# Kernel optimization log

Hardware: AMD Instinct MI355X
Metric: run time of the kernel (lower is better)

The kernel has to match this reference:

```python
import jax, jax.numpy as jnp
import numpy as np

B, C, D = 32, 24, 12          # batch, feature channels, spatial grid
Q_DIM = 11                    # hardcoded question dim in original (k*2+11)
K = C + 2                     # channels after coordinate concat
G_IN = 2 * K + Q_DIM          # 63
G_HID = 256
F_OUT = 10


def setup_inputs() -> dict:
    key = jax.random.key(0)
    ks = jax.random.split(key, 7)
    s = lambda fan_in: 1.0 / np.sqrt(fan_in)
    return {
        "image": jax.random.normal(ks[0], (B, C, D, D), jnp.float32),
        "question": jax.random.normal(ks[1], (B, Q_DIM), jnp.float32),
        "Wg1": jax.random.normal(ks[2], (G_IN, G_HID), jnp.float32) * s(G_IN),
        "bg1": jnp.zeros((G_HID,), jnp.float32),
        "Wg2": jax.random.normal(ks[3], (G_HID, G_HID), jnp.float32) * s(G_HID),
        "bg2": jnp.zeros((G_HID,), jnp.float32),
        "Wf1": jax.random.normal(ks[4], (G_HID, G_HID), jnp.float32) * s(G_HID),
        "bf1": jnp.zeros((G_HID,), jnp.float32),
        "Wf2": jax.random.normal(ks[5], (G_HID, F_OUT), jnp.float32) * s(G_HID),
        "bf2": jnp.zeros((F_OUT,), jnp.float32),
    }


def reference(image, question, Wg1, bg1, Wg2, bg2, Wf1, bf1, Wf2, bf2):
    b, c, d, _ = image.shape
    # coordinate channels: torch.arange(0, 1+1e-5, 1/(d-1)) == linspace(0,1,d)
    coord = jnp.linspace(0.0, 1.0, d, dtype=image.dtype)
    cx = jnp.broadcast_to(coord[None, None, None, :], (b, 1, d, d))
    cy = jnp.broadcast_to(coord[None, None, :, None], (b, 1, d, d))
    x = jnp.concatenate([image, cx, cy], axis=1)            # [b, k, d, d]
    k = c + 2
    n = d * d
    x = x.reshape(b, k, n).transpose(0, 2, 1)                # [b, n, k] objects
    # all-pairs construction: left repeats objects along axis 1, right along axis 2
    x_left = jnp.broadcast_to(x[:, None, :, :], (b, n, n, k)).reshape(b, n * n, k)
    x_right = jnp.broadcast_to(x[:, :, None, :], (b, n, n, k)).reshape(b, n * n, k)
    q = jnp.broadcast_to(question[:, None, :], (b, n * n, question.shape[1]))
    pairs = jnp.concatenate([x_left, x_right, q], axis=2)    # [b, n^2, 2k+11]
    # shared MLP g per pair
    h = jax.nn.relu(jnp.einsum('bpi,ih->bph', pairs, Wg1) + bg1)
    h = jax.nn.relu(jnp.einsum('bph,ho->bpo', h, Wg2) + bg2)
    s = h.sum(axis=1)                                        # [b, 256] sum over pairs
    # MLP f
    o = jax.nn.relu(s @ Wf1 + bf1)
    return o @ Wf2 + bf2                                     # [b, 10]
```

## Files before the change

kernel.cpp:

```cpp
#include <hip/hip_runtime.h>
#include <hip/hip_bf16.h>

#define NB   32
#define NC   24
#define ND   12
#define NN   144
#define QD   11
#define GH   256
#define FOUT 10

typedef unsigned short u16;
typedef __attribute__((ext_vector_type(8))) short bf16x8;
typedef __attribute__((ext_vector_type(4))) float f32x4;

#define LQ_U16  0
#define R_U16   1179648
#define BS_U16  2359296
#define S_BYTE  4849664

__device__ inline float b2f(u16 v) {
  union { unsigned u; float f; } c; c.u = ((unsigned)v) << 16; return c.f;
}
__device__ inline u16 f2b(float f) {
  __hip_bfloat16 h = __float2bfloat16(f);
  return *reinterpret_cast<u16*>(&h);
}

__global__ __launch_bounds__(256) void prep(const float* __restrict__ image,
                                            const float* __restrict__ question,
                                            const float* __restrict__ Wg1,
                                            const float* __restrict__ bg1,
                                            const float* __restrict__ Wg2,
                                            u16* __restrict__ Lq,
                                            u16* __restrict__ R,
                                            float* __restrict__ S,
                                            u16* __restrict__ Bswz) {
  int blk = blockIdx.x;
  int h   = threadIdx.x;
  if (blk < 2 * NB * NN) {
    int p     = blk % NN;
    int rest2 = blk / NN;
    int b     = rest2 & (NB - 1);
    int which = rest2 >> 5;
    const float* Wrow = Wg1 + which * (NC + 2) * GH;
    const float* img  = image + b * (NC * NN) + p;
    float acc = 0.f;
#pragma unroll
    for (int c = 0; c < NC; ++c) acc += img[c * NN] * Wrow[c * GH + h];
    int i = p / ND, j = p - i * ND;
    const float inv = 1.0f / (ND - 1);
    acc += (j * inv) * Wrow[24 * GH + h];
    acc += (i * inv) * Wrow[25 * GH + h];
    if (which == 0) {
      acc += bg1[h];
#pragma unroll
      for (int tq = 0; tq < QD; ++tq)
        acc += question[b * QD + tq] * Wg1[(2 * (NC + 2) + tq) * GH + h];
      Lq[(b * NN + p) * GH + h] = f2b(acc);
    } else {
      R[(b * NN + p) * GH + h] = f2b(acc);
    }
  } else {
    int tid = (blk - 2 * NB * NN) * 256 + h;
    int e   = tid & 7;
    int l   = (tid >> 3) & 63;
    int fid = tid >> 9;
    int kt  = fid >> 4, nt = fid & 15;
    int k = kt * 32 + ((l >> 4) << 3) + e;
    int n = (nt << 4) + (l & 15);
    Bswz[tid] = f2b(Wg2[k * GH + n]);
    if (tid < NB * GH) S[tid] = 0.f;
  }
}

__global__ __launch_bounds__(512, 2) void pair_gemm(const u16* __restrict__ Lq,
                                                    const u16* __restrict__ R,
                                                    const u16* __restrict__ Bswz,
                                                    const float* __restrict__ bg2,
                                                    float* __restrict__ S) {
  const int bid = blockIdx.x;
  const int xcd = bid & 7;
  const int idx = bid >> 3;
  const int b   = xcd * 4 + (idx >> 4);
  const int bi  = idx & 15;
  const int t0  = bi * 10 + (bi < 2 ? bi : 2);
  const int cnt = 10 + (bi < 2 ? 1 : 0);

  __shared__ __align__(16) u16 As[8 * 8 * 64 * 8];

  const int t = threadIdx.x;
  const int w = t >> 6, l = t & 63;
  const int wn = w & 3, wm = w >> 2;
  const int brow = t >> 2;
  const int oc   = t & 3;
  const int mf_w   = brow >> 4;
  const int lane_w = ((brow & 15) | (oc << 4)) ^ (oc << 1);
  const int lane_r = l ^ (((l >> 4) & 3) << 1);

  const u16* Lbase = Lq + b * NN * GH;
  const u16* Rbase = R + b * NN * GH;
  const u16* Bl    = Bswz + l * 8;

  float bgv[4];
#pragma unroll
  for (int nt = 0; nt < 4; ++nt)
    bgv[nt] = bg2[(wn << 6) + (nt << 4) + (l & 15)];
  float ssum[4] = {0.f, 0.f, 0.f, 0.f};

  for (int tt = 0; tt < cnt; ++tt) {
    {
      int p = (t0 + tt) * 128 + brow;
      int i = p / NN, j = p - i * NN;
      const u16* Lr = Lbase + i * GH + oc * 8;
      const u16* Rr = Rbase + j * GH + oc * 8;
#pragma unroll
      for (int half = 0; half < 2; ++half) {
        bf16x8 lv[4], rv[4];
#pragma unroll
        for (int q = 0; q < 4; ++q) {
          lv[q] = *(const bf16x8*)(Lr + ((half << 2) | q) * 32);
          rv[q] = *(const bf16x8*)(Rr + ((half << 2) | q) * 32);
        }
#pragma unroll
        for (int q = 0; q < 4; ++q) {
          const int kt = (half << 2) | q;
          u16 o[8];
#pragma unroll
          for (int e = 0; e < 8; ++e) {
            float v = b2f((u16)lv[q][e]) + b2f((u16)rv[q][e]);
            o[e] = f2b(v > 0.f ? v : 0.f);
          }
          *(bf16x8*)&As[((((kt << 3) | mf_w) << 6) | lane_w) << 3] =
              *(bf16x8*)o;
        }
      }
    }
    __syncthreads();

    f32x4 acc[4][4] = {};
#pragma unroll
    for (int kt = 0; kt < 8; ++kt) {
      bf16x8 af[4];
#pragma unroll
      for (int mf = 0; mf < 4; ++mf)
        af[mf] = *(const bf16x8*)
            &As[((((kt << 3) | (wm << 2) | mf) << 6) | lane_r) << 3];
      bf16x8 bfr[4];
#pragma unroll
      for (int nt = 0; nt < 4; ++nt) {
        int fid = (kt << 4) | (wn << 2) | nt;
        bfr[nt] = *(const bf16x8*)(Bl + ((size_t)fid << 9));
      }
      __builtin_amdgcn_s_setprio(1);
#pragma unroll
      for (int mf = 0; mf < 4; ++mf)
#pragma unroll
        for (int nt = 0; nt < 4; ++nt)
          acc[mf][nt] = __builtin_amdgcn_mfma_f32_16x16x32_bf16(
              af[mf], bfr[nt], acc[mf][nt], 0, 0, 0);
      __builtin_amdgcn_s_setprio(0);
    }
#pragma unroll
    for (int nt = 0; nt < 4; ++nt) {
      float s = 0.f;
#pragma unroll
      for (int mf = 0; mf < 4; ++mf)
#pragma unroll
        for (int r = 0; r < 4; ++r) {
          float v = acc[mf][nt][r] + bgv[nt];
          s += v > 0.f ? v : 0.f;
        }
      ssum[nt] += s;
    }
    __syncthreads();
  }

  float* Sb = S + b * GH;
#pragma unroll
  for (int nt = 0; nt < 4; ++nt) {
    float s = ssum[nt];
    s += __shfl_xor(s, 16, 64);
    s += __shfl_xor(s, 32, 64);
    if (l < 16) atomicAdd(&Sb[(wn << 6) + (nt << 4) + l], s);
  }
}

__global__ __launch_bounds__(256) void final_mlp(const float* __restrict__ S,
                                                 const float* __restrict__ Wf1,
                                                 const float* __restrict__ bf1,
                                                 const float* __restrict__ Wf2,
                                                 const float* __restrict__ bf2,
                                                 float* __restrict__ out) {
  __shared__ float sS[GH];
  __shared__ float oS[GH];
  int b = blockIdx.x, h = threadIdx.x;
  sS[h] = S[b * GH + h];
  __syncthreads();
  float acc = bf1[h];
#pragma unroll 8
  for (int k = 0; k < GH; ++k) acc += sS[k] * Wf1[k * GH + h];
  oS[h] = acc > 0.f ? acc : 0.f;
  __syncthreads();
  if (h < FOUT) {
    float o = bf2[h];
#pragma unroll 8
    for (int k = 0; k < GH; ++k) o += oS[k] * Wf2[k * FOUT + h];
    out[b * FOUT + h] = o;
  }
}

extern "C" void kernel_launch(void* const* d_in, const int* in_sizes, int n_in,
                              void* d_out, int out_size, void* d_ws, size_t ws_size,
                              hipStream_t stream) {
  const float* image    = (const float*)d_in[0];
  const float* question = (const float*)d_in[1];
  const float* Wg1      = (const float*)d_in[2];
  const float* bg1      = (const float*)d_in[3];
  const float* Wg2      = (const float*)d_in[4];
  const float* bg2      = (const float*)d_in[5];
  const float* Wf1      = (const float*)d_in[6];
  const float* bf1      = (const float*)d_in[7];
  const float* Wf2      = (const float*)d_in[8];
  const float* bf2      = (const float*)d_in[9];
  float* out = (float*)d_out;

  u16*   wsb  = (u16*)d_ws;
  u16*   Lqp  = wsb + LQ_U16;
  u16*   Rp   = wsb + R_U16;
  u16*   Bswz = wsb + BS_U16;
  float* Sp   = (float*)((char*)d_ws + S_BYTE);

  prep<<<2 * NB * NN + 256, 256, 0, stream>>>(image, question, Wg1, bg1, Wg2,
                                              Lqp, Rp, Sp, Bswz);
  pair_gemm<<<512, 512, 0, stream>>>(Lqp, Rp, Bswz, bg2, Sp);
  final_mlp<<<NB, 256, 0, stream>>>(Sp, Wf1, bf1, Wf2, bf2, out);
}
```

Before: 112.4 us.

## Switch pair GEMM to 32x32x16 MFMA with register-resident Wg2 fragments

Replaces the 16x16x32 MFMA tiling with 32x32x16 bf16 MFMA, so each wave keeps a 2x2 grid of 32x32 accumulators. Each wave's slice of the swizzled Wg2 is loaded once into registers instead of being re-read from global every tile. To match, the Wg2 swizzle layout and the LDS A-tile layout change, and the grid halves to 256 blocks that each process twice as many tiles. The aim is fewer B loads and higher MFMA efficiency, at the cost of much higher register pressure (occupancy 1 block per CU) and fewer blocks than CUs.

```diff
diff --git a/kernel.cpp b/kernel.cpp
--- a/kernel.cpp
+++ b/kernel.cpp
@@ -12,6 +12,7 @@
 typedef unsigned short u16;
 typedef __attribute__((ext_vector_type(8))) short bf16x8;
 typedef __attribute__((ext_vector_type(4))) float f32x4;
+typedef __attribute__((ext_vector_type(16))) float f32x16;
 
 #define LQ_U16  0
 #define R_U16   1179648
@@ -64,16 +65,16 @@
     int tid = (blk - 2 * NB * NN) * 256 + h;
     int e   = tid & 7;
     int l   = (tid >> 3) & 63;
-    int fid = tid >> 9;
-    int kt  = fid >> 4, nt = fid & 15;
-    int k = kt * 32 + ((l >> 4) << 3) + e;
-    int n = (nt << 4) + (l & 15);
+    int f   = tid >> 9;
+    int ks  = f >> 3, nf = f & 7;
+    int k = ks * 16 + ((l >> 5) << 3) + e;
+    int n = (nf << 5) + (l & 31);
     Bswz[tid] = f2b(Wg2[k * GH + n]);
     if (tid < NB * GH) S[tid] = 0.f;
   }
 }
 
-__global__ __launch_bounds__(512, 2) void pair_gemm(const u16* __restrict__ Lq,
+__global__ __launch_bounds__(512, 1) void pair_gemm(const u16* __restrict__ Lq,
                                                     const u16* __restrict__ R,
                                                     const u16* __restrict__ Bswz,
                                                     const float* __restrict__ bg2,
@@ -81,107 +82,104 @@
   const int bid = blockIdx.x;
   const int xcd = bid & 7;
   const int idx = bid >> 3;
-  const int b   = xcd * 4 + (idx >> 4);
-  const int bi  = idx & 15;
-  const int t0  = bi * 10 + (bi < 2 ? bi : 2);
-  const int cnt = 10 + (bi < 2 ? 1 : 0);
-
-  __shared__ __align__(16) u16 As[8 * 8 * 64 * 8];
+  const int b   = xcd * 4 + (idx >> 3);
+  const int bi  = idx & 7;
+  const int t0  = bi * 20 + (bi < 2 ? bi : 2);
+  const int cnt = 20 + (bi < 2 ? 1 : 0);
+
+  __shared__ __align__(16) u16 As[16 * 4 * 64 * 8];
 
   const int t = threadIdx.x;
   const int w = t >> 6, l = t & 63;
   const int wn = w & 3, wm = w >> 2;
   const int brow = t >> 2;
   const int oc   = t & 3;
-  const int mf_w   = brow >> 4;
-  const int lane_w = ((brow & 15) | (oc << 4)) ^ (oc << 1);
-  const int lane_r = l ^ (((l >> 4) & 3) << 1);
 
   const u16* Lbase = Lq + b * NN * GH;
   const u16* Rbase = R + b * NN * GH;
   const u16* Bl    = Bswz + l * 8;
 
-  float bgv[4];
-#pragma unroll
-  for (int nt = 0; nt < 4; ++nt)
-    bgv[nt] = bg2[(wn << 6) + (nt << 4) + (l & 15)];
-  float ssum[4] = {0.f, 0.f, 0.f, 0.f};
+  bf16x8 bq[2][16];
+#pragma unroll
+  for (int j = 0; j < 2; ++j)
+#pragma unroll
+    for (int ks = 0; ks < 16; ++ks)
+      bq[j][ks] = *(const bf16x8*)
+          (Bl + ((size_t)((ks << 3) | (wn << 1) | j) << 9));
+
+  float bgv[2];
+#pragma unroll
+  for (int j = 0; j < 2; ++j)
+    bgv[j] = bg2[(wn << 6) + (j << 5) + (l & 31)];
+  float ssum[2] = {0.f, 0.f};
 
   for (int tt = 0; tt < cnt; ++tt) {
     {
       int p = (t0 + tt) * 128 + brow;
       int i = p / NN, j = p - i * NN;
-      const u16* Lr = Lbase + i * GH + oc * 8;
-      const u16* Rr = Rbase + j * GH + oc * 8;
-#pragma unroll
-      for (int half = 0; half < 2; ++half) {
-        bf16x8 lv[4], rv[4];
-#pragma unroll
-        for (int q = 0; q < 4; ++q) {
-          lv[q] = *(const bf16x8*)(Lr + ((half << 2) | q) * 32);
-          rv[q] = *(const bf16x8*)(Rr + ((half << 2) | q) * 32);
+      const u16* Lr = Lbase + i * GH;
+      const u16* Rr = Rbase + j * GH;
+#pragma unroll
+      for (int u = 0; u < 8; ++u) {
+        const int ko = oc + (u << 2);
+        bf16x8 lv = *(const bf16x8*)(Lr + ko * 8);
+        bf16x8 rv = *(const bf16x8*)(Rr + ko * 8);
+        u16 o[8];
+#pragma unroll
+        for (int e = 0; e < 8; ++e) {
+          float v = b2f((u16)lv[e]) + b2f((u16)rv[e]);
+          o[e] = f2b(v > 0.f ? v : 0.f);
         }
-#pragma unroll
-        for (int q = 0; q < 4; ++q) {
-          const int kt = (half << 2) | q;
-          u16 o[8];
-#pragma unroll
-          for (int e = 0; e < 8; ++e) {
-            float v = b2f((u16)lv[q][e]) + b2f((u16)rv[q][e]);
-            o[e] = f2b(v > 0.f ? v : 0.f);
-          }
-          *(bf16x8*)&As[((((kt << 3) | mf_w) << 6) | lane_w) << 3] =
-              *(bf16x8*)o;
-        }
+        const int ks = ko >> 1;
+        const int kb = ko & 1;
+        const int mf = brow >> 5;
+        const int pl = ((kb << 5) | (brow & 31)) ^ (oc << 1);
+        *(bf16x8*)&As[((((ks << 2) | mf) << 6) | pl) << 3] = *(bf16x8*)o;
       }
     }
     __syncthreads();
 
-    f32x4 acc[4][4] = {};
-#pragma unroll
-    for (int kt = 0; kt < 8; ++kt) {
-      bf16x8 af[4];
-#pragma unroll
-      for (int mf = 0; mf < 4; ++mf)
-        af[mf] = *(const bf16x8*)
-            &As[((((kt << 3) | (wm << 2) | mf) << 6) | lane_r) << 3];
-      bf16x8 bfr[4];
-#pragma unroll
-      for (int nt = 0; nt < 4; ++nt) {
-        int fid = (kt << 4) | (wn << 2) | nt;
-        bfr[nt] = *(const bf16x8*)(Bl + ((size_t)fid << 9));
+    f32x16 acc[2][2] = {};
+#pragma unroll
+    for (int ks = 0; ks < 16; ++ks) {
+      bf16x8 af[2];
+#pragma unroll
+      for (int i = 0; i < 2; ++i) {
+        const int mf = (wm << 1) | i;
+        const int g  = ((((ks & 1) << 1) | (l >> 5)) << 1);
+        af[i] = *(const bf16x8*)&As[((((ks << 2) | mf) << 6) | (l ^ g)) << 3];
       }
       __builtin_amdgcn_s_setprio(1);
 #pragma unroll
-      for (int mf = 0; mf < 4; ++mf)
-#pragma unroll
-        for (int nt = 0; nt < 4; ++nt)
-          acc[mf][nt] = __builtin_amdgcn_mfma_f32_16x16x32_bf16(
-              af[mf], bfr[nt], acc[mf][nt], 0, 0, 0);
+      for (int i = 0; i < 2; ++i)
+#pragma unroll
+        for (int j = 0; j < 2; ++j)
+          acc[i][j] = __builtin_amdgcn_mfma_f32_32x32x16_bf16(
+              af[i], bq[j][ks], acc[i][j], 0, 0, 0);
       __builtin_amdgcn_s_setprio(0);
     }
-#pragma unroll
-    for (int nt = 0; nt < 4; ++nt) {
+
+#pragma unroll
+    for (int j = 0; j < 2; ++j) {
       float s = 0.f;
 #pragma unroll
-      for (int mf = 0; mf < 4; ++mf)
-#pragma unroll
-        for (int r = 0; r < 4; ++r) {
-          float v = acc[mf][nt][r] + bgv[nt];
+      for (int i = 0; i < 2; ++i)
+#pragma unroll
+        for (int r = 0; r < 16; ++r) {
+          float v = acc[i][j][r] + bgv[j];
           s += v > 0.f ? v : 0.f;
         }
-      ssum[nt] += s;
+      ssum[j] += s;
     }
     __syncthreads();
   }
 
   float* Sb = S + b * GH;
 #pragma unroll
-  for (int nt = 0; nt < 4; ++nt) {
-    float s = ssum[nt];
-    s += __shfl_xor(s, 16, 64);
+  for (int j = 0; j < 2; ++j) {
+    float s = ssum[j];
     s += __shfl_xor(s, 32, 64);
-    if (l < 16) atomicAdd(&Sb[(wn << 6) + (nt << 4) + l], s);
+    if (l < 32) atomicAdd(&Sb[(wn << 6) + (j << 5) + l], s);
   }
 }
 
@@ -232,6 +230,6 @@
 
   prep<<<2 * NB * NN + 256, 256, 0, stream>>>(image, question, Wg1, bg1, Wg2,
                                               Lqp, Rp, Sp, Bswz);
-  pair_gemm<<<512, 512, 0, stream>>>(Lqp, Rp, Bswz, bg2, Sp);
+  pair_gemm<<<256, 512, 0, stream>>>(Lqp, Rp, Bswz, bg2, Sp);
   final_mlp<<<NB, 256, 0, stream>>>(Sp, Wf1, bf1, Wf2, bf2, out);
 }
```

Result: slower. 118.0 us (+5.1%).

## Batch prep positions per block with register-held Wg1 rows; stagger pair_gemm starts

Applied to the files above, without the earlier changes.

The prep kernel shrinks from thousands of tiny blocks to 256 projection blocks. Each one loads its 26 Wg1 columns and the question/bias term into registers once, then loops over 36 spatial positions. This removes repeated weight reloads and per-block launch overhead, at the cost of less parallelism per block. Separately, half of the pair_gemm blocks now sleep briefly at startup, to stagger their initial global-memory bursts. That sleep adds idle time to those blocks.

```diff
diff --git a/kernel.cpp b/kernel.cpp
--- a/kernel.cpp
+++ b/kernel.cpp
@@ -37,31 +37,36 @@
                                             u16* __restrict__ Bswz) {
   int blk = blockIdx.x;
   int h   = threadIdx.x;
-  if (blk < 2 * NB * NN) {
-    int p     = blk % NN;
-    int rest2 = blk / NN;
-    int b     = rest2 & (NB - 1);
-    int which = rest2 >> 5;
-    const float* Wrow = Wg1 + which * (NC + 2) * GH;
-    const float* img  = image + b * (NC * NN) + p;
-    float acc = 0.f;
-#pragma unroll
-    for (int c = 0; c < NC; ++c) acc += img[c * NN] * Wrow[c * GH + h];
-    int i = p / ND, j = p - i * ND;
+  if (blk < 256) {
+    const int quarter = blk & 3;
+    const int b       = (blk >> 2) & 31;
+    const int which   = blk >> 7;
+    float Wl[NC + 2];
+#pragma unroll
+    for (int r = 0; r < NC + 2; ++r)
+      Wl[r] = Wg1[(which * (NC + 2) + r) * GH + h];
+    float qacc = 0.f;
+    if (which == 0) {
+      qacc = bg1[h];
+#pragma unroll
+      for (int tq = 0; tq < QD; ++tq)
+        qacc += question[b * QD + tq] * Wg1[(2 * (NC + 2) + tq) * GH + h];
+    }
+    const float* img = image + b * (NC * NN);
+    u16* dst = (which == 0 ? Lq : R) + b * NN * GH + h;
     const float inv = 1.0f / (ND - 1);
-    acc += (j * inv) * Wrow[24 * GH + h];
-    acc += (i * inv) * Wrow[25 * GH + h];
-    if (which == 0) {
-      acc += bg1[h];
-#pragma unroll
-      for (int tq = 0; tq < QD; ++tq)
-        acc += question[b * QD + tq] * Wg1[(2 * (NC + 2) + tq) * GH + h];
-      Lq[(b * NN + p) * GH + h] = f2b(acc);
-    } else {
-      R[(b * NN + p) * GH + h] = f2b(acc);
+#pragma unroll 4
+    for (int p = quarter * 36; p < quarter * 36 + 36; ++p) {
+      float acc = qacc;
+#pragma unroll
+      for (int c = 0; c < NC; ++c) acc += img[c * NN + p] * Wl[c];
+      int i = p / ND, j = p - i * ND;
+      acc += (j * inv) * Wl[24];
+      acc += (i * inv) * Wl[25];
+      dst[p * GH] = f2b(acc);
     }
   } else {
-    int tid = (blk - 2 * NB * NN) * 256 + h;
+    int tid = (blk - 256) * 256 + h;
     int e   = tid & 7;
     int l   = (tid >> 3) & 63;
     int fid = tid >> 9;
@@ -85,6 +90,8 @@
   const int bi  = idx & 15;
   const int t0  = bi * 10 + (bi < 2 ? bi : 2);
   const int cnt = 10 + (bi < 2 ? 1 : 0);
+
+  if (idx & 32) __builtin_amdgcn_s_sleep(94);
 
   __shared__ __align__(16) u16 As[8 * 8 * 64 * 8];
 
@@ -230,8 +237,8 @@
   u16*   Bswz = wsb + BS_U16;
   float* Sp   = (float*)((char*)d_ws + S_BYTE);
 
-  prep<<<2 * NB * NN + 256, 256, 0, stream>>>(image, question, Wg1, bg1, Wg2,
-                                              Lqp, Rp, Sp, Bswz);
+  prep<<<512, 256, 0, stream>>>(image, question, Wg1, bg1, Wg2,
+                                Lqp, Rp, Sp, Bswz);
   pair_gemm<<<512, 512, 0, stream>>>(Lqp, Rp, Bswz, bg2, Sp);
   final_mlp<<<NB, 256, 0, stream>>>(Sp, Wf1, bf1, Wf2, bf2, out);
 }
```

Result: no change. 110.6 us (-1.5%).
